# Kernel optimization log

Measured on AMD Instinct MI355X. Metric: run time of the kernel, lower is better.

## Reference

```python
import jax, jax.numpy as jnp
import numpy as np

B, C, H, W = 4, 256, 64, 64
CC = 32      # cond_channels
RATE = 2     # cond_downscale_rate
G = 8        # deformable_groups
K = 9        # 3x3 kernel positions
GN = 32      # GroupNorm groups
EPS = 1e-6


def conv2d(x, w, b, pad, groups=1):
    y = jax.lax.conv_general_dilated(x, w, (1, 1), [(pad, pad), (pad, pad)],
                                     feature_group_count=groups,
                                     dimension_numbers=('NCHW', 'OIHW', 'NCHW'))
    return y + b[None, :, None, None]


def group_norm(x, gamma, beta):
    b, c, h, w = x.shape
    xr = x.reshape(b, GN, c // GN, h, w)
    mu = xr.mean(axis=(2, 3, 4), keepdims=True)
    var = xr.var(axis=(2, 3, 4), keepdims=True)
    xn = ((xr - mu) * jax.lax.rsqrt(var + EPS)).reshape(b, c, h, w)
    return xn * gamma[None, :, None, None] + beta[None, :, None, None]


def bilinear_gather(img, y, x):
    # img [B,G,Cg,H,W]; y,x [B,G,Ho,Wo] -> [B,G,Cg,Ho,Wo], zeros outside
    Bb, Gg, Cg, Hh, Ww = img.shape
    Ho, Wo = y.shape[2], y.shape[3]
    y0 = jnp.floor(y); x0 = jnp.floor(x)
    wy1 = y - y0; wx1 = x - x0
    flat = img.reshape(Bb, Gg, Cg, Hh * Ww)

    def g(yi, xi):
        valid = (yi >= 0) & (yi <= Hh - 1) & (xi >= 0) & (xi <= Ww - 1)
        yc = jnp.clip(yi, 0, Hh - 1).astype(jnp.int32)
        xc = jnp.clip(xi, 0, Ww - 1).astype(jnp.int32)
        idx = (yc * Ww + xc).reshape(Bb, Gg, 1, Ho * Wo)
        v = jnp.take_along_axis(flat, jnp.broadcast_to(idx, (Bb, Gg, Cg, Ho * Wo)), axis=3)
        return v.reshape(Bb, Gg, Cg, Ho, Wo) * valid[:, :, None].astype(img.dtype)

    w00 = ((1 - wy1) * (1 - wx1))[:, :, None]
    w01 = ((1 - wy1) * wx1)[:, :, None]
    w10 = (wy1 * (1 - wx1))[:, :, None]
    w11 = (wy1 * wx1)[:, :, None]
    return w00 * g(y0, x0) + w01 * g(y0, x0 + 1) + w10 * g(y0 + 1, x0) + w11 * g(y0 + 1, x0 + 1)


def resize_bilinear(x, rate):
    # F.interpolate(..., mode='bilinear', align_corners=False), integer downscale
    b, c, h, w = x.shape
    ho, wo = h // rate, w // rate
    ys = (jnp.arange(ho, dtype=x.dtype) + 0.5) * rate - 0.5
    xs = (jnp.arange(wo, dtype=x.dtype) + 0.5) * rate - 0.5
    yy = jnp.broadcast_to(ys[:, None], (ho, wo))[None, None]
    xx = jnp.broadcast_to(xs[None, :], (ho, wo))[None, None]
    yy = jnp.broadcast_to(yy, (b, 1, ho, wo))
    xx = jnp.broadcast_to(xx, (b, 1, ho, wo))
    return bilinear_gather(x[:, None], yy, xx)[:, 0]


def deform_conv2d(x, offset, mask, w, b):
    # modulated deformable conv, 3x3, stride 1, pad 1 (torchvision semantics)
    Bb, Cin, Hh, Ww = x.shape
    Cg = Cin // G
    Cout = w.shape[0]
    xr = x.reshape(Bb, G, Cg, Hh, Ww)
    off = offset.reshape(Bb, G, K, 2, Hh, Ww)   # [..., (dy,dx), H, W]
    m = jax.nn.sigmoid(mask).reshape(Bb, G, K, Hh, Ww)
    base_y = jnp.arange(Hh, dtype=x.dtype)[:, None]
    base_x = jnp.arange(Ww, dtype=x.dtype)[None, :]
    acc = jnp.zeros((Bb, Cout, Hh, Ww), x.dtype)
    for k in range(K):
        kh, kw = k // 3 - 1, k % 3 - 1
        yy = base_y + kh + off[:, :, k, 0]
        xx = base_x + kw + off[:, :, k, 1]
        s = bilinear_gather(xr, yy, xx) * m[:, :, k][:, :, None]
        wk = w[:, :, kh + 1, kw + 1].reshape(Cout, G, Cg)
        acc = acc + jnp.einsum('bgchw,ogc->bohw', s, wk)
    return acc + b[None, :, None, None]


def setup_inputs() -> dict:
    key = jax.random.key(0)
    ks = jax.random.split(key, 8)
    d = {}
    d['x_main'] = jax.random.normal(ks[0], (B, C, H, W), jnp.float32)
    d['inpfeat'] = jax.random.normal(ks[1], (B, CC, H * RATE, W * RATE), jnp.float32)
    d['w1a'] = jax.random.normal(ks[2], (C, C + CC, 1, 1), jnp.float32) * (1.0 / np.sqrt(C + CC))
    d['b1a'] = jnp.zeros((C,), jnp.float32)
    d['g1'] = jnp.ones((C,), jnp.float32); d['be1'] = jnp.zeros((C,), jnp.float32)
    d['w1b'] = jax.random.normal(ks[3], (C, 1, 7, 7), jnp.float32) * (1.0 / 7.0)
    d['b1b'] = jnp.zeros((C,), jnp.float32)
    d['g2'] = jnp.ones((C,), jnp.float32); d['be2'] = jnp.zeros((C,), jnp.float32)
    d['w1c'] = jax.random.normal(ks[4], (C, C, 1, 1), jnp.float32) * (1.0 / np.sqrt(C))
    d['b1c'] = jnp.zeros((C,), jnp.float32)
    d['w2'] = jax.random.normal(ks[5], (C, C, 3, 3), jnp.float32) * (1.0 / np.sqrt(9 * C))
    d['b2'] = jnp.zeros((C,), jnp.float32)
    d['g3'] = jnp.ones((C,), jnp.float32); d['be3'] = jnp.zeros((C,), jnp.float32)
    d['w_off'] = jax.random.normal(ks[6], (3 * G * K, C, 3, 3), jnp.float32) * 0.01
    d['b_off'] = jnp.zeros((3 * G * K,), jnp.float32)
    d['w_dcn'] = jax.random.normal(ks[7], (C, C, 3, 3), jnp.float32) * (1.0 / np.sqrt(9 * C))
    d['b_dcn'] = jnp.zeros((C,), jnp.float32)
    return d


def reference(x_main, inpfeat, w1a, b1a, g1, be1, w1b, b1b, g2, be2, w1c, b1c,
              w2, b2, g3, be3, w_off, b_off, w_dcn, b_dcn):
    inp = resize_bilinear(inpfeat, RATE)                       # [B,CC,H,W]
    f = conv2d(jnp.concatenate([inp, x_main], axis=1), w1a, b1a, 0)
    f = jax.nn.silu(group_norm(f, g1, be1))
    f = conv2d(f, w1b, b1b, 3, groups=C)                       # depthwise 7x7
    f = jax.nn.silu(group_norm(f, g2, be2))
    f = conv2d(f, w1c, b1c, 0)
    off_feat = jax.nn.silu(group_norm(conv2d(f, w2, b2, 1), g3, be3))
    co = conv2d(off_feat, w_off, b_off, 1)                     # [B, 3*G*K, H, W]
    o1, o2, mk = jnp.split(co, 3, axis=1)
    offset = jnp.concatenate([o1, o2], axis=1)
    warp_feat = deform_conv2d(x_main, offset, mk, w_dcn, b_dcn)
    return warp_feat, off_feat
```

## Files before the change

### kernel.cpp

```cpp
#include <hip/hip_runtime.h>
#include <math.h>

constexpr int B = 4, C = 256, CC = 32, H = 64, W = 64, HW = H * W;
constexpr int G = 8, K = 9, GN = 32, CPG = C / GN;
constexpr int OFFC = 3 * G * K;

typedef __attribute__((ext_vector_type(8))) short short8;
typedef __attribute__((ext_vector_type(4))) float f32x4;

__device__ inline short f2bf(float f) {
  unsigned u = __builtin_bit_cast(unsigned, f);
  return (short)((u + 0x7FFFu + ((u >> 16) & 1u)) >> 16);
}
__device__ inline float bf2f(short s) {
  unsigned u = ((unsigned)(unsigned short)s) << 16;
  return __builtin_bit_cast(float, u);
}

__global__ void k_prep(const float* __restrict__ w1a, short* __restrict__ wT1a,
                       const float* __restrict__ w1c, short* __restrict__ wT1c,
                       const float* __restrict__ w2, short* __restrict__ wT2,
                       const float* __restrict__ woff, short* __restrict__ wToff,
                       const float* __restrict__ wdcn, short* __restrict__ wTd,
                       float* __restrict__ sbuf) {
  int id = blockIdx.x * 256 + threadIdx.x;
  if (id < 73728) {
    wT1a[id] = f2bf(w1a[id]);
  } else if (id < 139264) {
    int i = id - 73728;
    wT1c[i] = f2bf(w1c[i]);
  } else if (id < 204800) {
    int i = id - 139264;
    int o = i >> 8, ci = i & 255;
    #pragma unroll
    for (int k = 0; k < 9; ++k)
      wT2[((size_t)k * 256 + o) * 256 + ci] = f2bf(w2[(size_t)i * 9 + k]);
  } else if (id < 260096) {
    int i = id - 204800;
    int o = i / 256, ci = i % 256;
    #pragma unroll
    for (int k = 0; k < 9; ++k)
      wToff[((size_t)k * 216 + o) * 256 + ci] = f2bf(woff[(size_t)i * 9 + k]);
  } else if (id < 325632) {
    int i = id - 260096;
    int o = i >> 8, ci = i & 255;
    int g = ci >> 5, cg = ci & 31;
    #pragma unroll
    for (int k = 0; k < 9; ++k)
      wTd[(((size_t)g * 9 + k) * 256 + o) * 32 + cg] = f2bf(wdcn[(size_t)i * 9 + k]);
  } else if (id < 326400) {
    sbuf[id - 325632] = 0.f;
  }
}

__global__ void k_resizeT(const float* __restrict__ in, short* __restrict__ dst) {
  int t = threadIdx.x;
  int p0 = blockIdx.x * 64;
  int b = blockIdx.y;
  int px = t >> 2, cq = t & 3;
  int p = p0 + px;
  int y = p >> 6, x = p & 63;
  short8 v;
  #pragma unroll
  for (int j = 0; j < 8; ++j) {
    int c = cq * 8 + j;
    const float* src = in + ((size_t)b * CC + c) * (2 * H) * (2 * W) + (2 * y) * (2 * W) + 2 * x;
    v[j] = f2bf(0.25f * (src[0] + src[1] + src[2 * W] + src[2 * W + 1]));
  }
  *(short8*)(dst + ((size_t)b * HW + p) * 288 + cq * 8) = v;
}

__global__ void k_transpose(const float* __restrict__ src, short* __restrict__ dst,
                            int Csrc, int Cdst, int coff) {
  int t = threadIdx.x;
  int p0 = blockIdx.x * 64;
  int cc0 = blockIdx.y * 32;
  int b = blockIdx.z;
  int px = t >> 2, cq = t & 3;
  const float* s = src + ((size_t)b * Csrc + cc0 + cq * 8) * HW + p0 + px;
  short8 v;
  #pragma unroll
  for (int j = 0; j < 8; ++j) v[j] = f2bf(s[(size_t)j * HW]);
  *(short8*)(dst + ((size_t)b * HW + p0 + px) * Cdst + coff + cc0 + cq * 8) = v;
}

template<int CIN, int OUT_BF16>
__global__ __launch_bounds__(256) void k_conv1x1_mfma(
    const short* __restrict__ gT, const short* __restrict__ wT,
    const float* __restrict__ bias, void* __restrict__ outp) {
  const int tid = threadIdx.x;
  const int lane = tid & 63, wv = tid >> 6;
  const int l15 = lane & 15, l4 = lane >> 4;
  const int lin = blockIdx.x + gridDim.x * (blockIdx.y + gridDim.y * blockIdx.z);
  const int nb = gridDim.x * gridDim.y * gridDim.z;
  const int swz = (lin & 7) * (nb >> 3) + (lin >> 3);
  const int bx = swz % gridDim.x;
  const int rem = swz / gridDim.x;
  const int b = rem / gridDim.y;
  const int o0 = (rem % gridDim.y) * 64;
  const int p0 = bx * 128;

  const short* gTb = gT + (size_t)b * HW * CIN;
  const short* br[2];
  #pragma unroll
  for (int nt = 0; nt < 2; ++nt)
    br[nt] = gTb + (size_t)(p0 + wv * 32 + nt * 16 + l15) * CIN;
  const short* ar[4];
  #pragma unroll
  for (int mt = 0; mt < 4; ++mt)
    ar[mt] = wT + (size_t)(o0 + mt * 16 + l15) * CIN;

  f32x4 acc[4][2];
  #pragma unroll
  for (int mt = 0; mt < 4; ++mt)
    #pragma unroll
    for (int nt = 0; nt < 2; ++nt) acc[mt][nt] = (f32x4)0.f;

  short8 a_c[4], b_c[2], a_n[4], b_n[2];
  #pragma unroll
  for (int mt = 0; mt < 4; ++mt) a_c[mt] = *(const short8*)(ar[mt] + l4 * 8);
  #pragma unroll
  for (int nt = 0; nt < 2; ++nt) b_c[nt] = *(const short8*)(br[nt] + l4 * 8);

  for (int ck = 0; ck < CIN / 32; ++ck) {
    if (ck + 1 < CIN / 32) {
      int cin_n = (ck + 1) * 32 + l4 * 8;
      #pragma unroll
      for (int mt = 0; mt < 4; ++mt) a_n[mt] = *(const short8*)(ar[mt] + cin_n);
      #pragma unroll
      for (int nt = 0; nt < 2; ++nt) b_n[nt] = *(const short8*)(br[nt] + cin_n);
    }
    #pragma unroll
    for (int mt = 0; mt < 4; ++mt)
      #pragma unroll
      for (int nt = 0; nt < 2; ++nt)
        acc[mt][nt] = __builtin_amdgcn_mfma_f32_16x16x32_bf16(
            a_c[mt], b_c[nt], acc[mt][nt], 0, 0, 0);
    if (ck + 1 < CIN / 32) {
      #pragma unroll
      for (int mt = 0; mt < 4; ++mt) a_c[mt] = a_n[mt];
      #pragma unroll
      for (int nt = 0; nt < 2; ++nt) b_c[nt] = b_n[nt];
    }
  }

  #pragma unroll
  for (int mt = 0; mt < 4; ++mt) {
    #pragma unroll
    for (int nt = 0; nt < 2; ++nt) {
      int p = p0 + wv * 32 + nt * 16 + l15;
      if (OUT_BF16) {
        short4 vv;
        #pragma unroll
        for (int r = 0; r < 4; ++r) {
          int oo = o0 + mt * 16 + l4 * 4 + r;
          ((short*)&vv)[r] = f2bf(acc[mt][nt][r] + bias[oo]);
        }
        *(short4*)((short*)outp + ((size_t)b * HW + p) * 256 + o0 + mt * 16 + l4 * 4) = vv;
      } else {
        float* out = (float*)outp;
        #pragma unroll
        for (int r = 0; r < 4; ++r) {
          int oo = o0 + mt * 16 + l4 * 4 + r;
          out[((size_t)b * 256 + oo) * HW + p] = acc[mt][nt][r] + bias[oo];
        }
      }
    }
  }
}

template<int CIN, int COUT>
__global__ __launch_bounds__(256) void k_mfma_conv9(
    const short* __restrict__ gT, const short* __restrict__ wT,
    const float* __restrict__ bias, float* __restrict__ out) {
  constexpr int POS = 4 * 66;
  constexpr int PSTR = 40;
  constexpr int NCH = (POS * 4 + 255) / 256;
  __shared__ short lds[POS * PSTR];
  const int tid = threadIdx.x;
  const int lane = tid & 63, wv = tid >> 6;
  const int l15 = lane & 15, l4 = lane >> 4;
  const int lin = blockIdx.x + gridDim.x * (blockIdx.y + gridDim.y * blockIdx.z);
  const int nb = gridDim.x * gridDim.y * gridDim.z;
  const int swz = (lin & 7) * (nb >> 3) + (lin >> 3);
  const int bx = swz % gridDim.x;
  const int rem = swz / gridDim.x;
  const int b = rem / gridDim.y;
  const int o0 = (rem % gridDim.y) * 64;
  const int p0 = bx * 128;
  const int y0 = p0 >> 6;

  f32x4 acc[4][2];
  #pragma unroll
  for (int mt = 0; mt < 4; ++mt)
    #pragma unroll
    for (int nt = 0; nt < 2; ++nt) acc[mt][nt] = (f32x4)0.f;

  const short* gTb = gT + (size_t)b * HW * CIN;

  short8 pf[NCH];
  auto prefetch = [&](int ck) {
    const int ci0 = ck * 32;
    #pragma unroll
    for (int j = 0; j < NCH; ++j) {
      int i = tid + j * 256;
      if (i < POS * 4) {
        int pos = i >> 2, cq = i & 3;
        short8 v = {0, 0, 0, 0, 0, 0, 0, 0};
        int r = pos / 66;
        int cx = pos - r * 66 - 1;
        int y = y0 - 1 + r;
        if ((unsigned)y < (unsigned)H && (unsigned)cx < (unsigned)W)
          v = *(const short8*)(gTb + (size_t)(y * W + cx) * CIN + ci0 + cq * 8);
        pf[j] = v;
      }
    }
  };

  prefetch(0);
  for (int ck = 0; ck < CIN / 32; ++ck) {
    const int ci0 = ck * 32;
    __syncthreads();
    #pragma unroll
    for (int j = 0; j < NCH; ++j) {
      int i = tid + j * 256;
      if (i < POS * 4) {
        int pos = i >> 2, cq = i & 3;
        *(short8*)(lds + pos * PSTR + cq * 8) = pf[j];
      }
    }
    __syncthreads();
    if (ck + 1 < CIN / 32) prefetch(ck + 1);

    for (int tap = 0; tap < 9; ++tap) {
      short8 a[4];
      #pragma unroll
      for (int mt = 0; mt < 4; ++mt) {
        int o_r = o0 + mt * 16 + l15;
        if (COUT % 64 == 0 || o_r < COUT)
          a[mt] = *(const short8*)(wT + ((size_t)tap * COUT + o_r) * CIN + ci0 + l4 * 8);
        else
          a[mt] = (short8){0, 0, 0, 0, 0, 0, 0, 0};
      }
      short8 bb[2];
      #pragma unroll
      for (int nt = 0; nt < 2; ++nt) {
        int dy = tap / 3 - 1, dx = tap % 3 - 1;
        int row = (wv >> 1) + dy + 1;
        int col = (wv & 1) * 32 + nt * 16 + l15 + dx + 1;
        bb[nt] = *(const short8*)(lds + (row * 66 + col) * PSTR + l4 * 8);
      }
      #pragma unroll
      for (int mt = 0; mt < 4; ++mt)
        #pragma unroll
        for (int nt = 0; nt < 2; ++nt)
          acc[mt][nt] = __builtin_amdgcn_mfma_f32_16x16x32_bf16(
              a[mt], bb[nt], acc[mt][nt], 0, 0, 0);
    }
  }

  #pragma unroll
  for (int mt = 0; mt < 4; ++mt) {
    #pragma unroll
    for (int nt = 0; nt < 2; ++nt) {
      int p = p0 + wv * 32 + nt * 16 + l15;
      #pragma unroll
      for (int r = 0; r < 4; ++r) {
        int oo = o0 + mt * 16 + l4 * 4 + r;
        if (COUT % 64 == 0 || oo < COUT)
          out[((size_t)b * COUT + oo) * HW + p] = acc[mt][nt][r] + bias[oo];
      }
    }
  }
}

__global__ void k_gn_stats_part(const float* __restrict__ in,
                                float* __restrict__ ssum, float* __restrict__ ssq) {
  int g = blockIdx.x, b = blockIdx.y, z = blockIdx.z;
  const float4* base = (const float4*)(in + ((size_t)b * C + g * CPG) * HW) + z * 2048;
  float s = 0.f, s2 = 0.f;
  for (int i = threadIdx.x; i < 2048; i += 256) {
    float4 v = base[i];
    s  += v.x + v.y + v.z + v.w;
    s2 += v.x * v.x + v.y * v.y + v.z * v.z + v.w * v.w;
  }
  #pragma unroll
  for (int off = 32; off > 0; off >>= 1) {
    s  += __shfl_down(s, off);
    s2 += __shfl_down(s2, off);
  }
  __shared__ float sh[8];
  int wid = threadIdx.x >> 6, lane = threadIdx.x & 63;
  if (lane == 0) { sh[wid] = s; sh[4 + wid] = s2; }
  __syncthreads();
  if (threadIdx.x == 0) {
    atomicAdd(&ssum[b * GN + g], sh[0] + sh[1] + sh[2] + sh[3]);
    atomicAdd(&ssq[b * GN + g], sh[4] + sh[5] + sh[6] + sh[7]);
  }
}

template<int MODE>
__global__ void k_gnt(const float* __restrict__ in,
                      const float* __restrict__ ssum, const float* __restrict__ ssq,
                      const float* __restrict__ gamma, const float* __restrict__ beta,
                      short* __restrict__ T, float* __restrict__ outf) {
  int t = threadIdx.x;
  int p0 = blockIdx.x * 64;
  int b = blockIdx.y;
  int cc0 = blockIdx.z * 64;
  int px = t >> 2, cq = t & 3;
  int p = p0 + px;
  #pragma unroll
  for (int cc = 0; cc < 64; cc += 32) {
    int cbase = cc0 + cc + cq * 8;
    int bg = b * GN + (cbase >> 3);
    float mean = ssum[bg] * (1.f / (CPG * HW));
    float var  = ssq[bg] * (1.f / (CPG * HW)) - mean * mean;
    float inv  = rsqrtf(var + 1e-6f);
    short8 v;
    #pragma unroll
    for (int j = 0; j < 8; ++j) {
      int c = cbase + j;
      float x = in[((size_t)b * C + c) * HW + p];
      float y = (x - mean) * inv * gamma[c] + beta[c];
      y = y / (1.f + expf(-y));
      if (MODE >= 1) outf[((size_t)b * C + c) * HW + p] = y;
      v[j] = f2bf(y);
    }
    if (MODE != 2) *(short8*)(T + ((size_t)b * HW + p) * C + cbase) = v;
  }
}

__global__ void k_dw7(const float* __restrict__ in, const float* __restrict__ w,
                      const float* __restrict__ bias, float* __restrict__ out,
                      float* __restrict__ ssum, float* __restrict__ ssq) {
  int t = blockIdx.x * 256 + threadIdx.x;
  int c = blockIdx.y, b = blockIdx.z;
  int x4 = (t & 15) * 4;
  int y = t >> 4;
  const float* src = in + ((size_t)b * C + c) * HW;
  const float* wk = w + c * 49;
  float bz = bias[c];
  float a0 = bz, a1 = bz, a2 = bz, a3 = bz;
  const float4 z4 = make_float4(0.f, 0.f, 0.f, 0.f);
  #pragma unroll
  for (int ky = 0; ky < 7; ++ky) {
    int yy = y + ky - 3;
    if ((unsigned)yy >= (unsigned)H) continue;
    const float* row = src + yy * W;
    float4 A = (x4 >= 4)  ? *(const float4*)(row + x4 - 4) : z4;
    float4 Bm = *(const float4*)(row + x4);
    float4 Cx = (x4 <= 56) ? *(const float4*)(row + x4 + 4) : z4;
    float rb[12] = {A.x, A.y, A.z, A.w, Bm.x, Bm.y, Bm.z, Bm.w, Cx.x, Cx.y, Cx.z, Cx.w};
    #pragma unroll
    for (int kx = 0; kx < 7; ++kx) {
      float wv = wk[ky * 7 + kx];
      a0 += wv * rb[kx + 1];
      a1 += wv * rb[kx + 2];
      a2 += wv * rb[kx + 3];
      a3 += wv * rb[kx + 4];
    }
  }
  *(float4*)(out + ((size_t)b * C + c) * HW + y * W + x4) = make_float4(a0, a1, a2, a3);
  float s = a0 + a1 + a2 + a3;
  float s2 = a0 * a0 + a1 * a1 + a2 * a2 + a3 * a3;
  #pragma unroll
  for (int off = 32; off > 0; off >>= 1) {
    s  += __shfl_down(s, off);
    s2 += __shfl_down(s2, off);
  }
  __shared__ float sh[8];
  int wid = threadIdx.x >> 6, lane = threadIdx.x & 63;
  if (lane == 0) { sh[wid] = s; sh[4 + wid] = s2; }
  __syncthreads();
  if (threadIdx.x == 0) {
    atomicAdd(&ssum[b * GN + (c >> 3)], sh[0] + sh[1] + sh[2] + sh[3]);
    atomicAdd(&ssq[b * GN + (c >> 3)], sh[4] + sh[5] + sh[6] + sh[7]);
  }
}

__global__ __launch_bounds__(512, 4) void k_deform_mfma(
    const short* __restrict__ xmT, const float* __restrict__ co,
    const short* __restrict__ wT, const float* __restrict__ bias,
    float* __restrict__ out) {
  constexpr int PSTR = 40;
  __shared__ short s[2][K * 32 * PSTR];
  const int tid = threadIdx.x;
  const int lane = tid & 63, wv = tid >> 6;
  const int l15 = lane & 15, l4 = lane >> 4;
  const int lin = blockIdx.x + gridDim.x * blockIdx.y;
  const int nb = gridDim.x * gridDim.y;
  const int swz = (lin & 7) * (nb >> 3) + (lin >> 3);
  const int b = swz / (HW / 32);
  const int p0 = (swz % (HW / 32)) * 32;
  const bool producer = (wv >= 4);
  const int o0 = wv * 64;
  const int pid = tid - 256;

  const short* xb = xmT + (size_t)b * HW * C;
  const float* cob = co + (size_t)b * OFFC * HW;

  float cdy[5], cdx[5], cml[5];

  auto loadco = [&](int g) {
    #pragma unroll
    for (int j = 0; j < 5; ++j) {
      if (j == 4 && pid >= 128) continue;
      int i = pid + j * 256;
      int tap = i >> 7, pl = (i & 127) >> 2;
      int p = p0 + pl;
      cdy[j] = cob[(size_t)((g * K + tap) * 2) * HW + p];
      cdx[j] = cob[(size_t)((g * K + tap) * 2 + 1) * HW + p];
      cml[j] = cob[(size_t)(144 + g * K + tap) * HW + p];
    }
  };

  auto stage = [&](int g, short* sb) {
    #pragma unroll
    for (int j = 0; j < 5; ++j) {
      if (j == 4 && pid >= 128) continue;
      int i = pid + j * 256;
      int tap = i >> 7, r = i & 127, pl = r >> 2, cq = r & 3;
      int p = p0 + pl;
      float m = 1.f / (1.f + expf(-cml[j]));
      int kh = tap / 3 - 1, kw = tap % 3 - 1;
      int py = p >> 6, px = p & 63;
      float yy = (float)(py + kh) + cdy[j];
      float xx = (float)(px + kw) + cdx[j];
      float yf = floorf(yy), xf = floorf(xx);
      float wy = yy - yf, wx = xx - xf;
      int y0 = (int)yf, x0 = (int)xf;
      bool yv0 = (unsigned)y0 < (unsigned)H, yv1 = (unsigned)(y0 + 1) < (unsigned)H;
      bool xv0 = (unsigned)x0 < (unsigned)W, xv1 = (unsigned)(x0 + 1) < (unsigned)W;
      int yc0 = min(max(y0, 0), H - 1), yc1 = min(max(y0 + 1, 0), H - 1);
      int xc0 = min(max(x0, 0), W - 1), xc1 = min(max(x0 + 1, 0), W - 1);
      float w00 = (yv0 && xv0) ? (1.f - wy) * (1.f - wx) * m : 0.f;
      float w01 = (yv0 && xv1) ? (1.f - wy) * wx * m : 0.f;
      float w10 = (yv1 && xv0) ? wy * (1.f - wx) * m : 0.f;
      float w11 = (yv1 && xv1) ? wy * wx * m : 0.f;
      const short* xg = xb + g * 32 + cq * 8;
      short8 v00 = *(const short8*)(xg + (size_t)(yc0 * W + xc0) * C);
      short8 v01 = *(const short8*)(xg + (size_t)(yc0 * W + xc1) * C);
      short8 v10 = *(const short8*)(xg + (size_t)(yc1 * W + xc0) * C);
      short8 v11 = *(const short8*)(xg + (size_t)(yc1 * W + xc1) * C);
      short8 rr;
      #pragma unroll
      for (int jj = 0; jj < 8; ++jj)
        rr[jj] = f2bf(w00 * bf2f(v00[jj]) + w01 * bf2f(v01[jj]) +
                      w10 * bf2f(v10[jj]) + w11 * bf2f(v11[jj]));
      *(short8*)(sb + (tap * 32 + pl) * PSTR + cq * 8) = rr;
    }
  };

  f32x4 acc[4][2];
  #pragma unroll
  for (int mt = 0; mt < 4; ++mt)
    #pragma unroll
    for (int nt = 0; nt < 2; ++nt) acc[mt][nt] = (f32x4)0.f;

  if (producer) {
    loadco(0);
    stage(0, s[0]);
    loadco(1);
  }
  __syncthreads();
  for (int g = 0; g < G; ++g) {
    if (producer) {
      if (g < G - 1) {
        stage(g + 1, s[(g + 1) & 1]);
        if (g < G - 2) loadco(g + 2);
      }
    } else {
      const short* sb = s[g & 1];
      const short* wg = wT + (size_t)g * K * 256 * 32;
      short8 a_c[4], a_n[4];
      #pragma unroll
      for (int mt = 0; mt < 4; ++mt)
        a_c[mt] = *(const short8*)(wg + (size_t)(o0 + mt * 16 + l15) * 32 + l4 * 8);
      for (int k = 0; k < K; ++k) {
        short8 bb0 = *(const short8*)(sb + (k * 32 + l15) * PSTR + l4 * 8);
        short8 bb1 = *(const short8*)(sb + (k * 32 + 16 + l15) * PSTR + l4 * 8);
        if (k < K - 1) {
          #pragma unroll
          for (int mt = 0; mt < 4; ++mt)
            a_n[mt] = *(const short8*)(wg + (size_t)((k + 1) * 256 + o0 + mt * 16 + l15) * 32 + l4 * 8);
        }
        #pragma unroll
        for (int mt = 0; mt < 4; ++mt) {
          acc[mt][0] = __builtin_amdgcn_mfma_f32_16x16x32_bf16(a_c[mt], bb0, acc[mt][0], 0, 0, 0);
          acc[mt][1] = __builtin_amdgcn_mfma_f32_16x16x32_bf16(a_c[mt], bb1, acc[mt][1], 0, 0, 0);
        }
        if (k < K - 1) {
          #pragma unroll
          for (int mt = 0; mt < 4; ++mt) a_c[mt] = a_n[mt];
        }
      }
    }
    __syncthreads();
  }

  if (!producer) {
    #pragma unroll
    for (int mt = 0; mt < 4; ++mt) {
      #pragma unroll
      for (int nt = 0; nt < 2; ++nt) {
        int p = p0 + nt * 16 + l15;
        #pragma unroll
        for (int r = 0; r < 4; ++r) {
          int oo = o0 + mt * 16 + l4 * 4 + r;
          out[((size_t)b * C + oo) * HW + p] = acc[mt][nt][r] + bias[oo];
        }
      }
    }
  }
}

extern "C" void kernel_launch(void* const* d_in, const int* in_sizes, int n_in,
                              void* d_out, int out_size, void* d_ws, size_t ws_size,
                              hipStream_t stream) {
  const float* x_main  = (const float*)d_in[0];
  const float* inpfeat = (const float*)d_in[1];
  const float* w1a = (const float*)d_in[2];
  const float* b1a = (const float*)d_in[3];
  const float* g1  = (const float*)d_in[4];
  const float* be1 = (const float*)d_in[5];
  const float* w1b = (const float*)d_in[6];
  const float* b1b = (const float*)d_in[7];
  const float* g2  = (const float*)d_in[8];
  const float* be2 = (const float*)d_in[9];
  const float* w1c = (const float*)d_in[10];
  const float* b1c = (const float*)d_in[11];
  const float* w2  = (const float*)d_in[12];
  const float* b2  = (const float*)d_in[13];
  const float* g3  = (const float*)d_in[14];
  const float* be3 = (const float*)d_in[15];
  const float* w_off = (const float*)d_in[16];
  const float* b_off = (const float*)d_in[17];
  const float* w_dcn = (const float*)d_in[18];
  const float* b_dcn = (const float*)d_in[19];

  float* warp_out = (float*)d_out;
  float* off_out  = warp_out + (size_t)B * C * HW;

  char* ws = (char*)d_ws;
  float* r_inp = (float*)ws;
  float* fA    = (float*)(ws + (2u << 20));
  short* T288  = (short*)(ws + (2u << 20) + (16u << 20));
  char*  wbase = ws + (2u << 20) + (16u << 20) + 9437184;
  short* wT1a  = (short*)(wbase);
  short* wT1c  = (short*)(wbase + 147456);
  short* wT2   = (short*)(wbase + 147456 + 131072);
  short* wToff = (short*)(wbase + 147456 + 131072 + 1179648);
  float* sbuf  = (float*)(wbase + 147456 + 131072 + 1179648 + 995328);
  float* ssum1 = sbuf,       *ssq1 = sbuf + 128;
  float* ssum2 = sbuf + 256, *ssq2 = sbuf + 384;
  float* ssum3 = sbuf + 512, *ssq3 = sbuf + 640;
  short* wTd   = (short*)r_inp;
  short* Tc    = (short*)fA;
  short* T2    = T288;
  float* fB = warp_out;
  float* co = fA;

  k_prep<<<dim3(1275), 256, 0, stream>>>(w1a, wT1a, w1c, wT1c, w2, wT2,
                                         w_off, wToff, w_dcn, wTd, sbuf);
  k_resizeT<<<dim3(HW / 64, B), 256, 0, stream>>>(inpfeat, T288);
  k_transpose<<<dim3(HW / 64, 8, B), 256, 0, stream>>>(x_main, T288, C, 288, 32);
  k_conv1x1_mfma<288, 0><<<dim3(HW / 128, 4, B), 256, 0, stream>>>(T288, wT1a, b1a, fA);
  k_gn_stats_part<<<dim3(GN, B, 4), 256, 0, stream>>>(fA, ssum1, ssq1);
  k_gnt<2><<<dim3(HW / 64, B, 4), 256, 0, stream>>>(fA, ssum1, ssq1, g1, be1, nullptr, fA);
  k_dw7<<<dim3(HW / 1024, C, B), 256, 0, stream>>>(fA, w1b, b1b, fB, ssum2, ssq2);
  k_gnt<0><<<dim3(HW / 64, B, 4), 256, 0, stream>>>(fB, ssum2, ssq2, g2, be2, T2, nullptr);
  k_conv1x1_mfma<256, 1><<<dim3(HW / 128, 4, B), 256, 0, stream>>>(T2, wT1c, b1c, Tc);
  k_mfma_conv9<256, 256><<<dim3(HW / 128, 4, B), 256, 0, stream>>>(Tc, wT2, b2, fB);
  k_gn_stats_part<<<dim3(GN, B, 4), 256, 0, stream>>>(fB, ssum3, ssq3);
  k_gnt<1><<<dim3(HW / 64, B, 4), 256, 0, stream>>>(fB, ssum3, ssq3, g3, be3, T2, off_out);
  k_mfma_conv9<256, 216><<<dim3(HW / 128, 4, B), 256, 0, stream>>>(T2, wToff, b_off, co);
  k_transpose<<<dim3(HW / 64, 8, B), 256, 0, stream>>>(x_main, T288, C, 256, 0);
  k_deform_mfma<<<dim3(HW / 32, B), 512, 0, stream>>>(T288, co, wTd, b_dcn, warp_out);
}
```

Before: 347.2 us.

## Warp-specialize 3x3 MFMA conv with producer waves and double-buffered LDS

```diff
diff --git a/kernel.cpp b/kernel.cpp
--- a/kernel.cpp
+++ b/kernel.cpp
@@ -170,13 +170,12 @@
 }
 
 template<int CIN, int COUT>
-__global__ __launch_bounds__(256) void k_mfma_conv9(
+__global__ __launch_bounds__(512, 4) void k_mfma_conv9(
     const short* __restrict__ gT, const short* __restrict__ wT,
     const float* __restrict__ bias, float* __restrict__ out) {
   constexpr int POS = 4 * 66;
   constexpr int PSTR = 40;
-  constexpr int NCH = (POS * 4 + 255) / 256;
-  __shared__ short lds[POS * PSTR];
+  __shared__ short lds[2][POS * PSTR];
   const int tid = threadIdx.x;
   const int lane = tid & 63, wv = tid >> 6;
   const int l15 = lane & 15, l4 = lane >> 4;
@@ -189,21 +188,17 @@
   const int o0 = (rem % gridDim.y) * 64;
   const int p0 = bx * 128;
   const int y0 = p0 >> 6;
-
-  f32x4 acc[4][2];
-  #pragma unroll
-  for (int mt = 0; mt < 4; ++mt)
-    #pragma unroll
-    for (int nt = 0; nt < 2; ++nt) acc[mt][nt] = (f32x4)0.f;
+  const bool producer = (wv >= 4);
+  const int pid = tid - 256;
+  const int cwv = wv;
 
   const short* gTb = gT + (size_t)b * HW * CIN;
 
-  short8 pf[NCH];
-  auto prefetch = [&](int ck) {
+  auto stage = [&](int ck, short* sb) {
     const int ci0 = ck * 32;
     #pragma unroll
-    for (int j = 0; j < NCH; ++j) {
-      int i = tid + j * 256;
+    for (int j = 0; j < 5; ++j) {
+      int i = pid + j * 256;
       if (i < POS * 4) {
         int pos = i >> 2, cq = i & 3;
         short8 v = {0, 0, 0, 0, 0, 0, 0, 0};
@@ -212,63 +207,66 @@
         int y = y0 - 1 + r;
         if ((unsigned)y < (unsigned)H && (unsigned)cx < (unsigned)W)
           v = *(const short8*)(gTb + (size_t)(y * W + cx) * CIN + ci0 + cq * 8);
-        pf[j] = v;
+        *(short8*)(sb + pos * PSTR + cq * 8) = v;
       }
     }
   };
 
-  prefetch(0);
+  f32x4 acc[4][2];
+  #pragma unroll
+  for (int mt = 0; mt < 4; ++mt)
+    #pragma unroll
+    for (int nt = 0; nt < 2; ++nt) acc[mt][nt] = (f32x4)0.f;
+
+  if (producer) stage(0, lds[0]);
+  __syncthreads();
   for (int ck = 0; ck < CIN / 32; ++ck) {
-    const int ci0 = ck * 32;
+    if (producer) {
+      if (ck + 1 < CIN / 32) stage(ck + 1, lds[(ck + 1) & 1]);
+    } else {
+      const int ci0 = ck * 32;
+      const short* sb = lds[ck & 1];
+      for (int tap = 0; tap < 9; ++tap) {
+        short8 a[4];
+        #pragma unroll
+        for (int mt = 0; mt < 4; ++mt) {
+          int o_r = o0 + mt * 16 + l15;
+          if (COUT % 64 == 0 || o_r < COUT)
+            a[mt] = *(const short8*)(wT + ((size_t)tap * COUT + o_r) * CIN + ci0 + l4 * 8);
+          else
+            a[mt] = (short8){0, 0, 0, 0, 0, 0, 0, 0};
+        }
+        short8 bb[2];
+        #pragma unroll
+        for (int nt = 0; nt < 2; ++nt) {
+          int dy = tap / 3 - 1, dx = tap % 3 - 1;
+          int row = (cwv >> 1) + dy + 1;
+          int col = (cwv & 1) * 32 + nt * 16 + l15 + dx + 1;
+          bb[nt] = *(const short8*)(sb + (row * 66 + col) * PSTR + l4 * 8);
+        }
+        #pragma unroll
+        for (int mt = 0; mt < 4; ++mt)
+          #pragma unroll
+          for (int nt = 0; nt < 2; ++nt)
+            acc[mt][nt] = __builtin_amdgcn_mfma_f32_16x16x32_bf16(
+                a[mt], bb[nt], acc[mt][nt], 0, 0, 0);
+      }
+    }
     __syncthreads();
-    #pragma unroll
-    for (int j = 0; j < NCH; ++j) {
-      int i = tid + j * 256;
-      if (i < POS * 4) {
-        int pos = i >> 2, cq = i & 3;
-        *(short8*)(lds + pos * PSTR + cq * 8) = pf[j];
-      }
-    }
-    __syncthreads();
-    if (ck + 1 < CIN / 32) prefetch(ck + 1);
-
-    for (int tap = 0; tap < 9; ++tap) {
-      short8 a[4];
-      #pragma unroll
-      for (int mt = 0; mt < 4; ++mt) {
-        int o_r = o0 + mt * 16 + l15;
-        if (COUT % 64 == 0 || o_r < COUT)
-          a[mt] = *(const short8*)(wT + ((size_t)tap * COUT + o_r) * CIN + ci0 + l4 * 8);
-        else
-          a[mt] = (short8){0, 0, 0, 0, 0, 0, 0, 0};
-      }
-      short8 bb[2];
+  }
+
+  if (!producer) {
+    #pragma unroll
+    for (int mt = 0; mt < 4; ++mt) {
       #pragma unroll
       for (int nt = 0; nt < 2; ++nt) {
-        int dy = tap / 3 - 1, dx = tap % 3 - 1;
-        int row = (wv >> 1) + dy + 1;
-        int col = (wv & 1) * 32 + nt * 16 + l15 + dx + 1;
-        bb[nt] = *(const short8*)(lds + (row * 66 + col) * PSTR + l4 * 8);
-      }
-      #pragma unroll
-      for (int mt = 0; mt < 4; ++mt)
-        #pragma unroll
-        for (int nt = 0; nt < 2; ++nt)
-          acc[mt][nt] = __builtin_amdgcn_mfma_f32_16x16x32_bf16(
-              a[mt], bb[nt], acc[mt][nt], 0, 0, 0);
-    }
-  }
-
-  #pragma unroll
-  for (int mt = 0; mt < 4; ++mt) {
-    #pragma unroll
-    for (int nt = 0; nt < 2; ++nt) {
-      int p = p0 + wv * 32 + nt * 16 + l15;
-      #pragma unroll
-      for (int r = 0; r < 4; ++r) {
-        int oo = o0 + mt * 16 + l4 * 4 + r;
-        if (COUT % 64 == 0 || oo < COUT)
-          out[((size_t)b * COUT + oo) * HW + p] = acc[mt][nt][r] + bias[oo];
+        int p = p0 + cwv * 32 + nt * 16 + l15;
+        #pragma unroll
+        for (int r = 0; r < 4; ++r) {
+          int oo = o0 + mt * 16 + l4 * 4 + r;
+          if (COUT % 64 == 0 || oo < COUT)
+            out[((size_t)b * COUT + oo) * HW + p] = acc[mt][nt][r] + bias[oo];
+        }
       }
     }
   }
@@ -571,10 +569,10 @@
   k_dw7<<<dim3(HW / 1024, C, B), 256, 0, stream>>>(fA, w1b, b1b, fB, ssum2, ssq2);
   k_gnt<0><<<dim3(HW / 64, B, 4), 256, 0, stream>>>(fB, ssum2, ssq2, g2, be2, T2, nullptr);
   k_conv1x1_mfma<256, 1><<<dim3(HW / 128, 4, B), 256, 0, stream>>>(T2, wT1c, b1c, Tc);
-  k_mfma_conv9<256, 256><<<dim3(HW / 128, 4, B), 256, 0, stream>>>(Tc, wT2, b2, fB);
+  k_mfma_conv9<256, 256><<<dim3(HW / 128, 4, B), 512, 0, stream>>>(Tc, wT2, b2, fB);
   k_gn_stats_part<<<dim3(GN, B, 4), 256, 0, stream>>>(fB, ssum3, ssq3);
   k_gnt<1><<<dim3(HW / 64, B, 4), 256, 0, stream>>>(fB, ssum3, ssq3, g3, be3, T2, off_out);
-  k_mfma_conv9<256, 216><<<dim3(HW / 128, 4, B), 256, 0, stream>>>(T2, wToff, b_off, co);
+  k_mfma_conv9<256, 216><<<dim3(HW / 128, 4, B), 512, 0, stream>>>(T2, wToff, b_off, co);
   k_transpose<<<dim3(HW / 64, 8, B), 256, 0, stream>>>(x_main, T288, C, 256, 0);
   k_deform_mfma<<<dim3(HW / 32, B), 512, 0, stream>>>(T288, co, wTd, b_dcn, warp_out);
 }
```

Measured after the change: 347.6 us. Within noise of the previous version (+0.1%).

## Drop LDS staging in 3x3 MFMA conv and load activations directly from global

Applied to the files above, without the earlier changes.

```diff
diff --git a/kernel.cpp b/kernel.cpp
--- a/kernel.cpp
+++ b/kernel.cpp
@@ -173,10 +173,6 @@
 __global__ __launch_bounds__(256) void k_mfma_conv9(
     const short* __restrict__ gT, const short* __restrict__ wT,
     const float* __restrict__ bias, float* __restrict__ out) {
-  constexpr int POS = 4 * 66;
-  constexpr int PSTR = 40;
-  constexpr int NCH = (POS * 4 + 255) / 256;
-  __shared__ short lds[POS * PSTR];
   const int tid = threadIdx.x;
   const int lane = tid & 63, wv = tid >> 6;
   const int l15 = lane & 15, l4 = lane >> 4;
@@ -189,6 +185,11 @@
   const int o0 = (rem % gridDim.y) * 64;
   const int p0 = bx * 128;
   const int y0 = p0 >> 6;
+  const int rowb = y0 + (wv >> 1);
+  const int colb = (wv & 1) * 32 + l15;
+
+  const short* gTb = gT + (size_t)b * HW * CIN;
+  const short8 z8 = {0, 0, 0, 0, 0, 0, 0, 0};
 
   f32x4 acc[4][2];
   #pragma unroll
@@ -196,66 +197,38 @@
     #pragma unroll
     for (int nt = 0; nt < 2; ++nt) acc[mt][nt] = (f32x4)0.f;
 
-  const short* gTb = gT + (size_t)b * HW * CIN;
-
-  short8 pf[NCH];
-  auto prefetch = [&](int ck) {
-    const int ci0 = ck * 32;
-    #pragma unroll
-    for (int j = 0; j < NCH; ++j) {
-      int i = tid + j * 256;
-      if (i < POS * 4) {
-        int pos = i >> 2, cq = i & 3;
-        short8 v = {0, 0, 0, 0, 0, 0, 0, 0};
-        int r = pos / 66;
-        int cx = pos - r * 66 - 1;
-        int y = y0 - 1 + r;
-        if ((unsigned)y < (unsigned)H && (unsigned)cx < (unsigned)W)
-          v = *(const short8*)(gTb + (size_t)(y * W + cx) * CIN + ci0 + cq * 8);
-        pf[j] = v;
+  for (int ck = 0; ck < CIN / 32; ++ck) {
+    const int ci0 = ck * 32 + l4 * 8;
+    #pragma unroll
+    for (int tap = 0; tap < 9; ++tap) {
+      const int dy = tap / 3 - 1, dx = tap % 3 - 1;
+      const int row = rowb + dy;
+      if ((unsigned)row < (unsigned)H) {
+        short8 bb[2];
+        #pragma unroll
+        for (int nt = 0; nt < 2; ++nt) {
+          int col = colb + nt * 16 + dx;
+          bool v = (unsigned)col < (unsigned)W;
+          int cc = min(max(col, 0), W - 1);
+          short8 t = *(const short8*)(gTb + (size_t)(row * W + cc) * CIN + ci0);
+          bb[nt] = v ? t : z8;
+        }
+        short8 a[4];
+        #pragma unroll
+        for (int mt = 0; mt < 4; ++mt) {
+          int o_r = o0 + mt * 16 + l15;
+          if (COUT % 64 == 0 || o_r < COUT)
+            a[mt] = *(const short8*)(wT + ((size_t)tap * COUT + o_r) * CIN + ck * 32 + l4 * 8);
+          else
+            a[mt] = z8;
+        }
+        #pragma unroll
+        for (int mt = 0; mt < 4; ++mt)
+          #pragma unroll
+          for (int nt = 0; nt < 2; ++nt)
+            acc[mt][nt] = __builtin_amdgcn_mfma_f32_16x16x32_bf16(
+                a[mt], bb[nt], acc[mt][nt], 0, 0, 0);
       }
-    }
-  };
-
-  prefetch(0);
-  for (int ck = 0; ck < CIN / 32; ++ck) {
-    const int ci0 = ck * 32;
-    __syncthreads();
-    #pragma unroll
-    for (int j = 0; j < NCH; ++j) {
-      int i = tid + j * 256;
-      if (i < POS * 4) {
-        int pos = i >> 2, cq = i & 3;
-        *(short8*)(lds + pos * PSTR + cq * 8) = pf[j];
-      }
-    }
-    __syncthreads();
-    if (ck + 1 < CIN / 32) prefetch(ck + 1);
-
-    for (int tap = 0; tap < 9; ++tap) {
-      short8 a[4];
-      #pragma unroll
-      for (int mt = 0; mt < 4; ++mt) {
-        int o_r = o0 + mt * 16 + l15;
-        if (COUT % 64 == 0 || o_r < COUT)
-          a[mt] = *(const short8*)(wT + ((size_t)tap * COUT + o_r) * CIN + ci0 + l4 * 8);
-        else
-          a[mt] = (short8){0, 0, 0, 0, 0, 0, 0, 0};
-      }
-      short8 bb[2];
-      #pragma unroll
-      for (int nt = 0; nt < 2; ++nt) {
-        int dy = tap / 3 - 1, dx = tap % 3 - 1;
-        int row = (wv >> 1) + dy + 1;
-        int col = (wv & 1) * 32 + nt * 16 + l15 + dx + 1;
-        bb[nt] = *(const short8*)(lds + (row * 66 + col) * PSTR + l4 * 8);
-      }
-      #pragma unroll
-      for (int mt = 0; mt < 4; ++mt)
-        #pragma unroll
-        for (int nt = 0; nt < 2; ++nt)
-          acc[mt][nt] = __builtin_amdgcn_mfma_f32_16x16x32_bf16(
-              a[mt], bb[nt], acc[mt][nt], 0, 0, 0);
     }
   }
 
```

After: 402.1 us. 1.16x slower.
